# Optimization experiments

Measured on AMD Instinct MI355X. Metric: run time of the kernel, lower is better.

Reference implementation:

```python
import jax, jax.numpy as jnp
import numpy as np

N_NODES = 10000   # graph size (pos/field tables, dense adjacency)
FEATS = 32        # node_feats
HEADS = 4         # n_heads
SAMPLES = 256     # n_samples (random mids per endpoint)
SENTINELS = 8     # n_sentinels
N_BATCH = 2048    # edges per forward batch
N_EDGES_G = 100000  # graph edges used to build dense adjacency buffer


def setup_inputs() -> dict:
    key = jax.random.key(0)
    ks = jax.random.split(key, 7)
    edge = jax.random.randint(ks[0], (N_BATCH, 2), 0, N_NODES)
    mid0 = jax.random.randint(ks[1], (HEADS, N_BATCH, SAMPLES), 0, N_NODES)
    mid1 = jax.random.randint(ks[2], (HEADS, N_BATCH, SAMPLES), 0, N_NODES)
    # learned parameters (torch: nn.Parameter(torch.rand(...)), ones*5)
    pos = jax.random.uniform(ks[3], (HEADS, N_NODES, FEATS), dtype=jnp.float32)
    field = jax.random.uniform(ks[4], (HEADS, N_NODES, FEATS), dtype=jnp.float32)
    uncertainty = jnp.ones((1, 1, 1), jnp.float32) * 5.0
    # dense adjacency buffer: -1 everywhere, +1 on (symmetrized) graph edges
    src_g = jax.random.randint(ks[5], (N_EDGES_G,), 0, N_NODES)
    dst_g = jax.random.randint(ks[6], (N_EDGES_G,), 0, N_NODES)
    edge_mat = -jnp.ones((N_NODES, N_NODES), jnp.float32)
    edge_mat = edge_mat.at[src_g, dst_g].set(1.0).at[dst_g, src_g].set(1.0)
    return {"edge": edge, "mid0": mid0, "mid1": mid1, "pos": pos,
            "field": field, "uncertainty": uncertainty, "edge_mat": edge_mat}


def reference(edge, mid0, mid1, pos, field, uncertainty, edge_mat):
    src, dst = edge[:, 0], edge[:, 1]
    h = jnp.arange(HEADS)[:, None, None]           # head index for gathers
    # gather sampled mid-node positions and form difference vectors
    srcdiff = pos[:, src][:, :, None, :] - pos[h, mid0]   # (H, n, S, F)
    dstdiff = pos[:, dst][:, :, None, :] - pos[h, mid1]   # (H, n, S, F)
    # per-sample dot-product logits + memory bias (memory == -1 branch)
    logits1 = (jnp.einsum('hnsf,hnf->hns', srcdiff, field[:, dst])
               + uncertainty * edge_mat[mid0, dst[None, :, None]])
    logits2 = (jnp.einsum('hnsf,hnf->hns', dstdiff, field[:, src])
               + uncertainty * edge_mat[src[None, :, None], mid1])
    logits = jnp.concatenate([logits1, logits2], axis=2)  # (H, n, 2S)
    dist = jnp.concatenate([jnp.linalg.norm(srcdiff, axis=3),
                            jnp.linalg.norm(dstdiff, axis=3)], axis=2)
    # sentinels: zero logits at unit distance
    n = edge.shape[0]
    logits = jnp.concatenate([logits, jnp.zeros((HEADS, n, SENTINELS), logits.dtype)], axis=2)
    dist = jnp.concatenate([dist, jnp.ones((HEADS, n, SENTINELS), dist.dtype)], axis=2)
    # softmin aggregation: softmax over (1 - dist), weighted sum of logits, mean over heads
    w = jax.nn.softmax(1.0 - dist, axis=2)                # (H, n, 2S+sent)
    return jnp.sum(logits * w, axis=2).mean(0)            # (n,)
```

## Files before the change

### kernel.cpp

```cpp
#include <hip/hip_runtime.h>

#define N_NODES 10000
#define FEATS 32
#define HEADS 4
#define SAMPLES 256
#define N_BATCH 2048
#define NGROUP 40
#define NWORDS (NGROUP * 4)

__global__ __launch_bounds__(256) void mask_kernel(
    const int* __restrict__ edge,
    const float* __restrict__ edge_mat,
    unsigned long long* __restrict__ ws_mask,
    float* __restrict__ out)
{
    const int n    = blockIdx.x;
    const int tid  = threadIdx.x;
    const int wave = tid >> 6;
    const int lane = tid & 63;

    const int src = edge[2 * n];
    const int dst = edge[2 * n + 1];
    if (tid == 0) out[n] = 0.f;

    unsigned long long* wsn = ws_mask + (size_t)n * 2 * NWORDS;

    #pragma unroll
    for (int r = 0; r < 2; ++r) {
        const float* rp = edge_mat + (size_t)(r ? src : dst) * N_NODES;
        for (int g = wave; g < NGROUP; g += 4) {
            int base = g * 256 + lane * 4;
            float4 v = make_float4(-1.f, -1.f, -1.f, -1.f);
            if (base < N_NODES) v = *(const float4*)(rp + base);
            unsigned long long b0 = __ballot(v.x > 0.f);
            unsigned long long b1 = __ballot(v.y > 0.f);
            unsigned long long b2 = __ballot(v.z > 0.f);
            unsigned long long b3 = __ballot(v.w > 0.f);
            if (lane < 4) {
                unsigned long long b = lane == 0 ? b0 : lane == 1 ? b1
                                     : lane == 2 ? b2 : b3;
                wsn[r * NWORDS + g * 4 + lane] = b;
            }
        }
    }
}

__global__ __launch_bounds__(256) void madgraph_kernel(
    const int* __restrict__ edge,
    const int* __restrict__ mid0,
    const int* __restrict__ mid1,
    const float* __restrict__ pos,
    const float* __restrict__ field,
    const float* __restrict__ unc,
    const unsigned long long* __restrict__ ws_mask,
    float* __restrict__ out)
{
    const int b    = blockIdx.x;
    const int h    = b & 3;
    const int tid  = threadIdx.x;
    const int w    = tid >> 6;
    const int lane = tid & 63;
    const int n    = (b >> 2) + 512 * w;

    __shared__ unsigned long long s_mask[4][2 * NWORDS];

    const int src = edge[2 * n];
    const int dst = edge[2 * n + 1];
    const float U = unc[0];

    const unsigned long long* wsn = ws_mask + (size_t)n * 2 * NWORDS;
    #pragma unroll
    for (int k = 0; k < 5; ++k)
        s_mask[w][k * 64 + lane] = wsn[k * 64 + lane];

    const float* posh   = pos   + (size_t)h * N_NODES * FEATS;
    const float* fieldh = field + (size_t)h * N_NODES * FEATS;

    const int q = lane & 3;
    const int g = lane >> 2;

    float4 A[2][2], F[2][2];
    #pragma unroll
    for (int sd = 0; sd < 2; ++sd) {
        const float4* pa = (const float4*)(posh   + (size_t)(sd ? dst : src) * FEATS);
        const float4* pf = (const float4*)(fieldh + (size_t)(sd ? src : dst) * FEATS);
        A[sd][0] = pa[q];
        A[sd][1] = pa[q + 4];
        F[sd][0] = pf[q];
        F[sd][1] = pf[q + 4];
    }

    const size_t sb = ((size_t)h * N_BATCH + n) * SAMPLES;
    int mm[8];
    #pragma unroll
    for (int c = 0; c < 8; ++c)
        mm[c] = (c < 4 ? mid0 : mid1)[sb + (c & 3) * 64 + lane];

    float num = 0.f, den = 0.f;

    #pragma unroll
    for (int c = 0; c < 8; ++c) {
        const int side = c >> 2;
        #pragma unroll
        for (int t = 0; t < 4; ++t) {
            const int m = __shfl(mm[c], t * 16 + g);
            const float4* rp = (const float4*)(posh + (size_t)m * FEATS);
            float4 b0 = rp[q];
            float4 b1 = rp[q + 4];

            float dh = 0.f, nh = 0.f;
            {
                float4 a = A[side][0], f = F[side][0];
                float dx = a.x - b0.x, dy = a.y - b0.y,
                      dz = a.z - b0.z, dw = a.w - b0.w;
                dh += dx * f.x + dy * f.y + dz * f.z + dw * f.w;
                nh += dx * dx + dy * dy + dz * dz + dw * dw;
            }
            {
                float4 a = A[side][1], f = F[side][1];
                float dx = a.x - b1.x, dy = a.y - b1.y,
                      dz = a.z - b1.z, dw = a.w - b1.w;
                dh += dx * f.x + dy * f.y + dz * f.z + dw * f.w;
                nh += dx * dx + dy * dy + dz * dz + dw * dw;
            }
            dh += __shfl_xor(dh, 1); nh += __shfl_xor(nh, 1);
            dh += __shfl_xor(dh, 2); nh += __shfl_xor(nh, 2);

            const unsigned long long wbits =
                s_mask[w][side * NWORDS + ((m >> 8) << 2) + (m & 3)];
            const float em = ((wbits >> ((m >> 2) & 63)) & 1ull) ? U : -U;

            const float wgt = __expf(1.0f - sqrtf(nh));
            num += (dh + em) * wgt;
            den += wgt;
        }
    }

    #pragma unroll
    for (int off = 32; off > 0; off >>= 1) {
        num += __shfl_xor(num, off);
        den += __shfl_xor(den, off);
    }
    if (lane == 0) {
        atomicAdd(out + n, 0.25f * (num / (den + 32.0f)));
    }
}

extern "C" void kernel_launch(void* const* d_in, const int* in_sizes, int n_in,
                              void* d_out, int out_size, void* d_ws, size_t ws_size,
                              hipStream_t stream) {
    const int*   edge     = (const int*)  d_in[0];
    const int*   mid0     = (const int*)  d_in[1];
    const int*   mid1     = (const int*)  d_in[2];
    const float* pos      = (const float*)d_in[3];
    const float* field    = (const float*)d_in[4];
    const float* unc      = (const float*)d_in[5];
    const float* edge_mat = (const float*)d_in[6];
    float*       out      = (float*)d_out;
    unsigned long long* ws_mask = (unsigned long long*)d_ws;

    mask_kernel<<<N_BATCH, 256, 0, stream>>>(edge, edge_mat, ws_mask, out);
    madgraph_kernel<<<N_BATCH, 256, 0, stream>>>(edge, mid0, mid1, pos,
                                                 field, unc, ws_mask, out);
}
```

Baseline: 64.50 us.

## Fuse adjacency mask build into main kernel with one block per edge

Merges the mask-building kernel into the main kernel. Each block now handles one edge, building the two adjacency-row bitmasks in shared memory and then having its four waves process the four heads. The per-head atomics are replaced by a shared-memory reduction and a single plain store, and the edge_mat rows are read with nontemporal loads. This removes a kernel launch, the workspace round trip and the output zeroing. In exchange the bitmask build and the gather work now run serially inside each block, with an extra barrier.

```diff
diff --git a/kernel.cpp b/kernel.cpp
--- a/kernel.cpp
+++ b/kernel.cpp
@@ -8,71 +8,52 @@
 #define NGROUP 40
 #define NWORDS (NGROUP * 4)
 
-__global__ __launch_bounds__(256) void mask_kernel(
-    const int* __restrict__ edge,
-    const float* __restrict__ edge_mat,
-    unsigned long long* __restrict__ ws_mask,
-    float* __restrict__ out)
-{
-    const int n    = blockIdx.x;
-    const int tid  = threadIdx.x;
-    const int wave = tid >> 6;
-    const int lane = tid & 63;
+typedef float f32x4 __attribute__((ext_vector_type(4)));
 
-    const int src = edge[2 * n];
-    const int dst = edge[2 * n + 1];
-    if (tid == 0) out[n] = 0.f;
-
-    unsigned long long* wsn = ws_mask + (size_t)n * 2 * NWORDS;
-
-    #pragma unroll
-    for (int r = 0; r < 2; ++r) {
-        const float* rp = edge_mat + (size_t)(r ? src : dst) * N_NODES;
-        for (int g = wave; g < NGROUP; g += 4) {
-            int base = g * 256 + lane * 4;
-            float4 v = make_float4(-1.f, -1.f, -1.f, -1.f);
-            if (base < N_NODES) v = *(const float4*)(rp + base);
-            unsigned long long b0 = __ballot(v.x > 0.f);
-            unsigned long long b1 = __ballot(v.y > 0.f);
-            unsigned long long b2 = __ballot(v.z > 0.f);
-            unsigned long long b3 = __ballot(v.w > 0.f);
-            if (lane < 4) {
-                unsigned long long b = lane == 0 ? b0 : lane == 1 ? b1
-                                     : lane == 2 ? b2 : b3;
-                wsn[r * NWORDS + g * 4 + lane] = b;
-            }
-        }
-    }
-}
-
-__global__ __launch_bounds__(256) void madgraph_kernel(
+__global__ __launch_bounds__(256) void madgraph_fused(
     const int* __restrict__ edge,
     const int* __restrict__ mid0,
     const int* __restrict__ mid1,
     const float* __restrict__ pos,
     const float* __restrict__ field,
     const float* __restrict__ unc,
-    const unsigned long long* __restrict__ ws_mask,
+    const float* __restrict__ edge_mat,
     float* __restrict__ out)
 {
-    const int b    = blockIdx.x;
-    const int h    = b & 3;
+    const int n    = blockIdx.x;
     const int tid  = threadIdx.x;
     const int w    = tid >> 6;
     const int lane = tid & 63;
-    const int n    = (b >> 2) + 512 * w;
 
-    __shared__ unsigned long long s_mask[4][2 * NWORDS];
+    __shared__ unsigned long long s_mask[2 * NWORDS];
+    __shared__ float s_num[HEADS], s_den[HEADS];
 
     const int src = edge[2 * n];
     const int dst = edge[2 * n + 1];
     const float U = unc[0];
 
-    const unsigned long long* wsn = ws_mask + (size_t)n * 2 * NWORDS;
     #pragma unroll
-    for (int k = 0; k < 5; ++k)
-        s_mask[w][k * 64 + lane] = wsn[k * 64 + lane];
+    for (int r = 0; r < 2; ++r) {
+        const float* rp = edge_mat + (size_t)(r ? src : dst) * N_NODES;
+        for (int g = w; g < NGROUP; g += HEADS) {
+            int base = g * 256 + lane * 4;
+            f32x4 v = {-1.f, -1.f, -1.f, -1.f};
+            if (base < N_NODES)
+                v = __builtin_nontemporal_load((const f32x4*)(rp + base));
+            unsigned long long b0 = __ballot(v.x > 0.f);
+            unsigned long long b1 = __ballot(v.y > 0.f);
+            unsigned long long b2 = __ballot(v.z > 0.f);
+            unsigned long long b3 = __ballot(v.w > 0.f);
+            if (lane < 4) {
+                unsigned long long bb = lane == 0 ? b0 : lane == 1 ? b1
+                                      : lane == 2 ? b2 : b3;
+                s_mask[r * NWORDS + g * 4 + lane] = bb;
+            }
+        }
+    }
+    __syncthreads();
 
+    const int h = w;
     const float* posh   = pos   + (size_t)h * N_NODES * FEATS;
     const float* fieldh = field + (size_t)h * N_NODES * FEATS;
 
@@ -127,7 +108,7 @@
             dh += __shfl_xor(dh, 2); nh += __shfl_xor(nh, 2);
 
             const unsigned long long wbits =
-                s_mask[w][side * NWORDS + ((m >> 8) << 2) + (m & 3)];
+                s_mask[side * NWORDS + ((m >> 8) << 2) + (m & 3)];
             const float em = ((wbits >> ((m >> 2) & 63)) & 1ull) ? U : -U;
 
             const float wgt = __expf(1.0f - sqrtf(nh));
@@ -141,8 +122,15 @@
         num += __shfl_xor(num, off);
         den += __shfl_xor(den, off);
     }
-    if (lane == 0) {
-        atomicAdd(out + n, 0.25f * (num / (den + 32.0f)));
+    if (lane == 0) { s_num[w] = num; s_den[w] = den; }
+    __syncthreads();
+
+    if (tid == 0) {
+        float acc = 0.f;
+        #pragma unroll
+        for (int hh = 0; hh < HEADS; ++hh)
+            acc += s_num[hh] / (s_den[hh] + 32.0f);
+        out[n] = 0.25f * acc;
     }
 }
 
@@ -157,9 +145,7 @@
     const float* unc      = (const float*)d_in[5];
     const float* edge_mat = (const float*)d_in[6];
     float*       out      = (float*)d_out;
-    unsigned long long* ws_mask = (unsigned long long*)d_ws;
 
-    mask_kernel<<<N_BATCH, 256, 0, stream>>>(edge, edge_mat, ws_mask, out);
-    madgraph_kernel<<<N_BATCH, 256, 0, stream>>>(edge, mid0, mid1, pos,
-                                                 field, unc, ws_mask, out);
+    madgraph_fused<<<N_BATCH, 256, 0, stream>>>(edge, mid0, mid1, pos, field,
+                                                unc, edge_mat, out);
 }
```

Result: slower. 75.91 us (+17.7%).
